# Kernel optimization log

Hardware: AMD Instinct MI355X
Metric: run time of the kernel (lower is better)

The kernel has to match this reference:

```python
import jax, jax.numpy as jnp
import numpy as np

NUM_NODES = 50000
FEAT_DIM = 64
HIDDEN = 128
OUT_DIM = 128
NUM_EDGES = 640000


def setup_inputs() -> dict:
    key = jax.random.key(0)
    ks = jax.random.split(key, 8)
    edge_index = jax.random.randint(ks[0], (2, NUM_EDGES), 0, NUM_NODES, dtype=jnp.int32)
    emb = jax.random.normal(ks[1], (NUM_NODES, FEAT_DIM), dtype=jnp.float32) * 0.1
    # SAGEConv: lin_l (aggregated neighbors, with bias) and lin_r (root, no bias)
    s1 = 1.0 / np.sqrt(FEAT_DIM)
    W1l = jax.random.uniform(ks[2], (HIDDEN, FEAT_DIM), jnp.float32, -s1, s1)
    b1l = jnp.zeros((HIDDEN,), jnp.float32)
    W1r = jax.random.uniform(ks[3], (HIDDEN, FEAT_DIM), jnp.float32, -s1, s1)
    s2 = 1.0 / np.sqrt(HIDDEN)
    W2l = jax.random.uniform(ks[4], (OUT_DIM, HIDDEN), jnp.float32, -s2, s2)
    b2l = jnp.zeros((OUT_DIM,), jnp.float32)
    W2r = jax.random.uniform(ks[5], (OUT_DIM, HIDDEN), jnp.float32, -s2, s2)
    return {"edge_index": edge_index, "emb": emb, "W1l": W1l, "b1l": b1l,
            "W1r": W1r, "W2l": W2l, "b2l": b2l, "W2r": W2r}


def _sage_conv(x, src, dst, Wl, bl, Wr):
    # mean-aggregate source features at target nodes, then two linear paths
    msg = x[src]                                   # [E, d]
    agg = jax.ops.segment_sum(msg, dst, num_segments=NUM_NODES)
    deg = jax.ops.segment_sum(jnp.ones((src.shape[0],), x.dtype), dst,
                              num_segments=NUM_NODES)
    mean = agg / jnp.maximum(deg, 1.0)[:, None]    # [N, d]
    return mean @ Wl.T + bl + x @ Wr.T             # [N, out]


def reference(edge_index, emb, W1l, b1l, W1r, W2l, b2l, W2r):
    src, dst = edge_index[0], edge_index[1]
    h = jax.nn.relu(_sage_conv(emb, src, dst, W1l, b1l, W1r))
    return _sage_conv(h, src, dst, W2l, b2l, W2r)
```

## Files before the change

### kernel.cpp

```cpp
#include <hip/hip_runtime.h>

#define N_NODES 50000
#define FEAT    64
#define HID     128
#define N_EDGES 640000
#define NBLK    196
#define GCAP    64

typedef __attribute__((ext_vector_type(8))) short bf16x8;
typedef __attribute__((ext_vector_type(4))) float f32x4;

static __device__ __forceinline__ unsigned short f2bf(float f) {
    unsigned u = __float_as_uint(f);
    u = u + 0x7fffu + ((u >> 16) & 1u);
    return (unsigned short)(u >> 16);
}
static __device__ __forceinline__ float bflo(unsigned u) {
    return __uint_as_float(u << 16);
}
static __device__ __forceinline__ float bfhi(unsigned u) {
    return __uint_as_float(u & 0xffff0000u);
}

#define ACC8(A, v) { \
    A[0] += bflo((v).x); A[1] += bfhi((v).x); \
    A[2] += bflo((v).y); A[3] += bfhi((v).y); \
    A[4] += bflo((v).z); A[5] += bfhi((v).z); \
    A[6] += bflo((v).w); A[7] += bfhi((v).w); }

static __device__ __forceinline__ void gridbar(int* bar, int gen) {
    __syncthreads();
    if (threadIdx.x == 0) {
        __threadfence();
        int arrived = atomicAdd(&bar[0], 1);
        if (arrived == NBLK - 1) {
            atomicExch(&bar[0], 0);
            __threadfence();
            atomicExch(&bar[1], gen);
        } else {
            while (atomicAdd(&bar[1], 0) < gen) __builtin_amdgcn_s_sleep(2);
        }
        __threadfence();
    }
    __syncthreads();
}

__global__ __launch_bounds__(256) void histcvt_kernel(
        const int* __restrict__ dst, const float* __restrict__ emb,
        const float* __restrict__ W1l, const float* __restrict__ W1r,
        const float* __restrict__ W2l, const float* __restrict__ W2r,
        int* __restrict__ count, int* __restrict__ eslot,
        unsigned* __restrict__ emb_bf_u, unsigned* __restrict__ Wbf_u,
        unsigned* __restrict__ hbf_u) {
    int gtid = blockIdx.x * 256 + threadIdx.x;
    if (gtid < N_EDGES) {
        int slot = atomicAdd(&count[dst[gtid]], 1);
        eslot[gtid] = slot;
    }
    for (int i = gtid; i < N_NODES * FEAT / 2; i += N_EDGES) {
        float2 v = ((const float2*)emb)[i];
        emb_bf_u[i] = ((unsigned)f2bf(v.y) << 16) | (unsigned)f2bf(v.x);
    }
    if (gtid < FEAT / 2) emb_bf_u[N_NODES * FEAT / 2 + gtid] = 0u;
    if (gtid < HID / 2)  hbf_u[N_NODES * HID / 2 + gtid]   = 0u;
    if (gtid < 24576) {
        int w = gtid * 2;
        float lo, hi;
        if (w < 8192)       { lo = W1l[w];         hi = W1l[w + 1]; }
        else if (w < 16384) { lo = W1r[w - 8192];  hi = W1r[w - 8191]; }
        else if (w < 32768) { lo = W2l[w - 16384]; hi = W2l[w - 16383]; }
        else                { lo = W2r[w - 32768]; hi = W2r[w - 32767]; }
        Wbf_u[gtid] = ((unsigned)f2bf(hi) << 16) | (unsigned)f2bf(lo);
    }
}

__global__ __launch_bounds__(256) void scanperm_kernel(
        const int* __restrict__ count, int* offset, int* dhist, int* dcur,
        int* bsum, int* boff, int* dstart, int* perm, int* bar) {
    __shared__ int tmp[256];
    __shared__ int lh[64];
    __shared__ int lb2[64];
    int t = threadIdx.x;
    int gtid = blockIdx.x * 256 + t;

    {
        if (t < 64) lh[t] = 0;
        int v = (gtid < N_NODES) ? count[gtid] : 0;
        tmp[t] = v;
        __syncthreads();
        if (gtid < N_NODES) atomicAdd(&lh[v < 63 ? v : 63], 1);
        for (int off = 1; off < 256; off <<= 1) {
            int add = (t >= off) ? tmp[t - off] : 0;
            __syncthreads();
            tmp[t] += add;
            __syncthreads();
        }
        if (gtid < N_NODES) offset[gtid] = tmp[t] - v;
        if (t == 255) bsum[blockIdx.x] = tmp[255];
        if (t < 64 && lh[t] > 0) atomicAdd(&dhist[t], lh[t]);
    }
    gridbar(bar, 1);

    if (blockIdx.x < 2) {
        const int* in  = (blockIdx.x == 0) ? bsum : dhist;
        int*       out = (blockIdx.x == 0) ? boff : dstart;
        int cnt        = (blockIdx.x == 0) ? NBLK : 64;
        int v = (t < cnt) ? in[t] : 0;
        tmp[t] = v;
        __syncthreads();
        for (int off = 1; off < 256; off <<= 1) {
            int add = (t >= off) ? tmp[t - off] : 0;
            __syncthreads();
            tmp[t] += add;
            __syncthreads();
        }
        if (t < cnt) out[t] = tmp[t] - v;
    }
    gridbar(bar, 2);

    if (gtid < N_NODES) offset[gtid] += boff[blockIdx.x];
    if (gtid == 0) offset[N_NODES] = N_EDGES;
    {
        if (t < 64) lh[t] = 0;
        __syncthreads();
        int d = 0, slot = 0;
        if (gtid < N_NODES) {
            int c = count[gtid];
            d = c < 63 ? c : 63;
            slot = atomicAdd(&lh[d], 1);
        }
        __syncthreads();
        if (t < 64 && lh[t] > 0) lb2[t] = atomicAdd(&dcur[t], lh[t]);
        __syncthreads();
        if (gtid < N_NODES)
            perm[(N_NODES - 1) - (dstart[d] + lb2[d] + slot)] = gtid;
    }
}

__global__ void fill_kernel(const int* __restrict__ src, const int* __restrict__ dst,
                            const int* __restrict__ offset,
                            const int* __restrict__ eslot, int* __restrict__ esrc) {
    int e = blockIdx.x * blockDim.x + threadIdx.x;
    if (e >= N_EDGES) return;
    esrc[offset[dst[e]] + eslot[e]] = src[e];
}

__global__ __launch_bounds__(256, 4) void fgemm1_kernel(
        const unsigned short* __restrict__ embb, const int* __restrict__ offset,
        const int* __restrict__ esrc, const int* __restrict__ perm,
        const short* __restrict__ Wl, const short* __restrict__ Wr,
        const float* __restrict__ bias, unsigned short* __restrict__ hout) {
    __shared__ unsigned short smean[16][72];
    __shared__ int sidx[16][GCAP];
    __shared__ int nid[16];
    int t = threadIdx.x;
    if (t < 16) nid[t] = perm[blockIdx.x * 16 + t];
    __syncthreads();

    int sub = t >> 4, fl = t & 15;
    int half = (t >> 3) & 1, fo = t & 7;
    int n = nid[sub];
    int beg = offset[n], deg = offset[n + 1] - beg;
    bool fast = deg <= GCAP;
    int rr = (deg + 15) & ~15;
    if (fast) {
        for (int j = fl; j < rr; j += 16)
            sidx[sub][j] = (j < deg) ? esrc[beg + j] : N_NODES;
    }
    float acc[8] = {0,0,0,0,0,0,0,0};
    const uint4* eb4 = (const uint4*)embb;
    if (fast) {
        for (int i = 0; i < rr; i += 16) {
            uint4 v0 = eb4[(size_t)sidx[sub][i +  0 + half] * 8 + fo];
            uint4 v1 = eb4[(size_t)sidx[sub][i +  2 + half] * 8 + fo];
            uint4 v2 = eb4[(size_t)sidx[sub][i +  4 + half] * 8 + fo];
            uint4 v3 = eb4[(size_t)sidx[sub][i +  6 + half] * 8 + fo];
            uint4 v4 = eb4[(size_t)sidx[sub][i +  8 + half] * 8 + fo];
            uint4 v5 = eb4[(size_t)sidx[sub][i + 10 + half] * 8 + fo];
            uint4 v6 = eb4[(size_t)sidx[sub][i + 12 + half] * 8 + fo];
            uint4 v7 = eb4[(size_t)sidx[sub][i + 14 + half] * 8 + fo];
            ACC8(acc, v0) ACC8(acc, v1) ACC8(acc, v2) ACC8(acc, v3)
            ACC8(acc, v4) ACC8(acc, v5) ACC8(acc, v6) ACC8(acc, v7)
        }
    } else {
        for (int i = half; i < deg; i += 2) {
            uint4 v = eb4[(size_t)esrc[beg + i] * 8 + fo];
            ACC8(acc, v)
        }
    }
    float dinv = 1.0f / fmaxf((float)deg, 1.0f);
    unsigned ow[4];
    #pragma unroll
    for (int k = 0; k < 4; ++k) {
        float lo = acc[2 * k];     lo += __shfl_xor(lo, 8);
        float hi = acc[2 * k + 1]; hi += __shfl_xor(hi, 8);
        ow[k] = ((unsigned)f2bf(hi * dinv) << 16) | (unsigned)f2bf(lo * dinv);
    }
    if (half == 0) {
        uint4 o4 = {ow[0], ow[1], ow[2], ow[3]};
        *(uint4*)&smean[sub][fo * 8] = o4;
    }
    __syncthreads();

    int wave = t >> 6, lane = t & 63;
    int col = lane & 15, quad = lane >> 4;
    int ncol = nid[col];
    int nt0 = wave * 2, nt1 = nt0 + 1;
    f32x4 acc0 = (f32x4){0.f,0.f,0.f,0.f}, acc1 = (f32x4){0.f,0.f,0.f,0.f};
    #pragma unroll
    for (int kb = 0; kb < FEAT; kb += 32) {
        bf16x8 am = *(const bf16x8*)&smean[col][kb + quad * 8];
        bf16x8 ax = *(const bf16x8*)(embb + (size_t)ncol * FEAT + kb + quad * 8);
        bf16x8 bl0 = *(const bf16x8*)(Wl + (nt0 * 16 + col) * FEAT + kb + quad * 8);
        bf16x8 br0 = *(const bf16x8*)(Wr + (nt0 * 16 + col) * FEAT + kb + quad * 8);
        bf16x8 bl1 = *(const bf16x8*)(Wl + (nt1 * 16 + col) * FEAT + kb + quad * 8);
        bf16x8 br1 = *(const bf16x8*)(Wr + (nt1 * 16 + col) * FEAT + kb + quad * 8);
        acc0 = __builtin_amdgcn_mfma_f32_16x16x32_bf16(am, bl0, acc0, 0, 0, 0);
        acc0 = __builtin_amdgcn_mfma_f32_16x16x32_bf16(ax, br0, acc0, 0, 0, 0);
        acc1 = __builtin_amdgcn_mfma_f32_16x16x32_bf16(am, bl1, acc1, 0, 0, 0);
        acc1 = __builtin_amdgcn_mfma_f32_16x16x32_bf16(ax, br1, acc1, 0, 0, 0);
    }
    float bv0 = bias[nt0 * 16 + col];
    float bv1 = bias[nt1 * 16 + col];
    #pragma unroll
    for (int r = 0; r < 4; ++r) {
        int node = nid[quad * 4 + r];
        hout[(size_t)node * HID + nt0 * 16 + col] = f2bf(fmaxf(acc0[r] + bv0, 0.f));
        hout[(size_t)node * HID + nt1 * 16 + col] = f2bf(fmaxf(acc1[r] + bv1, 0.f));
    }
}

__global__ __launch_bounds__(256, 4) void fgemm2_kernel(
        const unsigned short* __restrict__ hbf, const int* __restrict__ offset,
        const int* __restrict__ esrc, const int* __restrict__ perm,
        const short* __restrict__ Wl, const short* __restrict__ Wr,
        const float* __restrict__ bias, float* __restrict__ out) {
    __shared__ unsigned short smean[16][136];
    __shared__ int sidx[16][GCAP];
    __shared__ int nid[16];
    int t = threadIdx.x;
    if (t < 16) nid[t] = perm[blockIdx.x * 16 + t];
    __syncthreads();

    int sub = t >> 4, fl = t & 15;
    int n = nid[sub];
    int beg = offset[n], deg = offset[n + 1] - beg;
    bool fast = deg <= GCAP;
    int rr = (deg + 7) & ~7;
    if (fast) {
        for (int j = fl; j < rr; j += 16)
            sidx[sub][j] = (j < deg) ? esrc[beg + j] : N_NODES;
    }
    float acc[8] = {0,0,0,0,0,0,0,0};
    const uint4* hb4 = (const uint4*)hbf;
    if (fast) {
        for (int i = 0; i < rr; i += 8) {
            uint4 v0 = hb4[(size_t)sidx[sub][i + 0] * 16 + fl];
            uint4 v1 = hb4[(size_t)sidx[sub][i + 1] * 16 + fl];
            uint4 v2 = hb4[(size_t)sidx[sub][i + 2] * 16 + fl];
            uint4 v3 = hb4[(size_t)sidx[sub][i + 3] * 16 + fl];
            uint4 v4 = hb4[(size_t)sidx[sub][i + 4] * 16 + fl];
            uint4 v5 = hb4[(size_t)sidx[sub][i + 5] * 16 + fl];
            uint4 v6 = hb4[(size_t)sidx[sub][i + 6] * 16 + fl];
            uint4 v7 = hb4[(size_t)sidx[sub][i + 7] * 16 + fl];
            ACC8(acc, v0) ACC8(acc, v1) ACC8(acc, v2) ACC8(acc, v3)
            ACC8(acc, v4) ACC8(acc, v5) ACC8(acc, v6) ACC8(acc, v7)
        }
    } else {
        for (int i = 0; i < deg; ++i) {
            uint4 v = hb4[(size_t)esrc[beg + i] * 16 + fl];
            ACC8(acc, v)
        }
    }
    float dinv = 1.0f / fmaxf((float)deg, 1.0f);
    unsigned ow[4];
    #pragma unroll
    for (int k = 0; k < 4; ++k) {
        float lo = acc[2 * k] * dinv;
        float hi = acc[2 * k + 1] * dinv;
        ow[k] = ((unsigned)f2bf(hi) << 16) | (unsigned)f2bf(lo);
    }
    uint4 o4 = {ow[0], ow[1], ow[2], ow[3]};
    *(uint4*)&smean[sub][fl * 8] = o4;
    __syncthreads();

    int wave = t >> 6, lane = t & 63;
    int col = lane & 15, quad = lane >> 4;
    int ncol = nid[col];
    int nt0 = wave * 2, nt1 = nt0 + 1;
    f32x4 acc0 = (f32x4){0.f,0.f,0.f,0.f}, acc1 = (f32x4){0.f,0.f,0.f,0.f};
    #pragma unroll
    for (int kb = 0; kb < HID; kb += 32) {
        bf16x8 am = *(const bf16x8*)&smean[col][kb + quad * 8];
        bf16x8 ax = *(const bf16x8*)(hbf + (size_t)ncol * HID + kb + quad * 8);
        bf16x8 bl0 = *(const bf16x8*)(Wl + (nt0 * 16 + col) * HID + kb + quad * 8);
        bf16x8 br0 = *(const bf16x8*)(Wr + (nt0 * 16 + col) * HID + kb + quad * 8);
        bf16x8 bl1 = *(const bf16x8*)(Wl + (nt1 * 16 + col) * HID + kb + quad * 8);
        bf16x8 br1 = *(const bf16x8*)(Wr + (nt1 * 16 + col) * HID + kb + quad * 8);
        acc0 = __builtin_amdgcn_mfma_f32_16x16x32_bf16(am, bl0, acc0, 0, 0, 0);
        acc0 = __builtin_amdgcn_mfma_f32_16x16x32_bf16(ax, br0, acc0, 0, 0, 0);
        acc1 = __builtin_amdgcn_mfma_f32_16x16x32_bf16(am, bl1, acc1, 0, 0, 0);
        acc1 = __builtin_amdgcn_mfma_f32_16x16x32_bf16(ax, br1, acc1, 0, 0, 0);
    }
    float bv0 = bias[nt0 * 16 + col];
    float bv1 = bias[nt1 * 16 + col];
    #pragma unroll
    for (int r = 0; r < 4; ++r) {
        int node = nid[quad * 4 + r];
        out[(size_t)node * HID + nt0 * 16 + col] = acc0[r] + bv0;
        out[(size_t)node * HID + nt1 * 16 + col] = acc1[r] + bv1;
    }
}

extern "C" void kernel_launch(void* const* d_in, const int* in_sizes, int n_in,
                              void* d_out, int out_size, void* d_ws, size_t ws_size,
                              hipStream_t stream) {
    const int*   edge_index = (const int*)d_in[0];
    const float* emb        = (const float*)d_in[1];
    const float* W1l        = (const float*)d_in[2];
    const float* b1l        = (const float*)d_in[3];
    const float* W1r        = (const float*)d_in[4];
    const float* W2l        = (const float*)d_in[5];
    const float* b2l        = (const float*)d_in[6];
    const float* W2r        = (const float*)d_in[7];
    float* out = (float*)d_out;

    const int* src = edge_index;
    const int* dst = edge_index + N_EDGES;

    int* iws    = (int*)d_ws;
    int* offset = iws;
    int* count  = iws + 50004;
    int* dhist  = iws + 100004;
    int* dcur   = iws + 100068;
    int* bar    = iws + 100132;
    int* bsum   = iws + 100136;
    int* boff   = iws + 100392;
    int* dstart = iws + 100648;
    int* perm   = iws + 100712;
    int* esrc   = iws + 150712;
    int* eslot  = iws + 790712;
    unsigned short* W1l_bf = (unsigned short*)(iws + 1430712);
    unsigned short* W1r_bf = (unsigned short*)(iws + 1434808);
    unsigned short* W2l_bf = (unsigned short*)(iws + 1438904);
    unsigned short* W2r_bf = (unsigned short*)(iws + 1447096);
    unsigned short* Wbf    = W1l_bf;
    unsigned short* emb_bf = (unsigned short*)(iws + 1455288);
    unsigned short* hbf    = (unsigned short*)(iws + 3055320);

    (void)hipMemsetAsync(count, 0, (size_t)(100136 - 50004) * sizeof(int), stream);

    histcvt_kernel<<<(N_EDGES + 255) / 256, 256, 0, stream>>>(
        dst, emb, W1l, W1r, W2l, W2r, count, eslot,
        (unsigned*)emb_bf, (unsigned*)Wbf, (unsigned*)hbf);
    scanperm_kernel<<<NBLK, 256, 0, stream>>>(
        count, offset, dhist, dcur, bsum, boff, dstart, perm, bar);
    fill_kernel<<<(N_EDGES + 255) / 256, 256, 0, stream>>>(
        src, dst, offset, eslot, esrc);

    fgemm1_kernel<<<N_NODES / 16, 256, 0, stream>>>(
        emb_bf, offset, esrc, perm,
        (const short*)W1l_bf, (const short*)W1r_bf, b1l, hbf);
    fgemm2_kernel<<<N_NODES / 16, 256, 0, stream>>>(
        hbf, offset, esrc, perm,
        (const short*)W2l_bf, (const short*)W2r_bf, b2l, out);
}
```

Before: 230.5 us.

## Double-buffer neighbor gathers through LDS with async global_load_lds in both layers

Replaces the register-based unrolled neighbor gather in both fused SAGE kernels with a two-stage pipeline. It issues asynchronous global_load_lds transfers into a per-wave LDS staging buffer, waits with explicit vmcnt, and accumulates from LDS while the next batch is in flight. The fast-path decision now uses the wave-wide maximum degree, so all 16-lane groups in a wave share one loop trip count. The aim is to keep more gather loads outstanding and hide memory latency. The cost is extra LDS usage, manual waitcnt handling that could be fragile, and wasted padded loads when a wave's degrees are uneven.

```diff
diff --git a/kernel.cpp b/kernel.cpp
--- a/kernel.cpp
+++ b/kernel.cpp
@@ -27,6 +27,12 @@
     A[2] += bflo((v).y); A[3] += bfhi((v).y); \
     A[4] += bflo((v).z); A[5] += bfhi((v).z); \
     A[6] += bflo((v).w); A[7] += bfhi((v).w); }
+
+typedef __attribute__((address_space(1))) const void glob_void;
+typedef __attribute__((address_space(3))) void lds_void;
+static __device__ __forceinline__ void gload16(const void* g, void* l) {
+    __builtin_amdgcn_global_load_lds((glob_void*)g, (lds_void*)l, 16, 0, 0);
+}
 
 static __device__ __forceinline__ void gridbar(int* bar, int gen) {
     __syncthreads();
@@ -153,35 +159,60 @@
     __shared__ unsigned short smean[16][72];
     __shared__ int sidx[16][GCAP];
     __shared__ int nid[16];
+    __shared__ uint4 stg[4][2][4][4][2][8];
     int t = threadIdx.x;
     if (t < 16) nid[t] = perm[blockIdx.x * 16 + t];
     __syncthreads();
 
     int sub = t >> 4, fl = t & 15;
+    int w = t >> 6;
+    int subloc = sub & 3;
     int half = (t >> 3) & 1, fo = t & 7;
     int n = nid[sub];
     int beg = offset[n], deg = offset[n + 1] - beg;
-    bool fast = deg <= GCAP;
-    int rr = (deg + 15) & ~15;
-    if (fast) {
-        for (int j = fl; j < rr; j += 16)
-            sidx[sub][j] = (j < deg) ? esrc[beg + j] : N_NODES;
-    }
+    int degw = deg;
+    degw = max(degw, __shfl_xor(degw, 16));
+    degw = max(degw, __shfl_xor(degw, 32));
     float acc[8] = {0,0,0,0,0,0,0,0};
     const uint4* eb4 = (const uint4*)embb;
-    if (fast) {
-        for (int i = 0; i < rr; i += 16) {
-            uint4 v0 = eb4[(size_t)sidx[sub][i +  0 + half] * 8 + fo];
-            uint4 v1 = eb4[(size_t)sidx[sub][i +  2 + half] * 8 + fo];
-            uint4 v2 = eb4[(size_t)sidx[sub][i +  4 + half] * 8 + fo];
-            uint4 v3 = eb4[(size_t)sidx[sub][i +  6 + half] * 8 + fo];
-            uint4 v4 = eb4[(size_t)sidx[sub][i +  8 + half] * 8 + fo];
-            uint4 v5 = eb4[(size_t)sidx[sub][i + 10 + half] * 8 + fo];
-            uint4 v6 = eb4[(size_t)sidx[sub][i + 12 + half] * 8 + fo];
-            uint4 v7 = eb4[(size_t)sidx[sub][i + 14 + half] * 8 + fo];
-            ACC8(acc, v0) ACC8(acc, v1) ACC8(acc, v2) ACC8(acc, v3)
-            ACC8(acc, v4) ACC8(acc, v5) ACC8(acc, v6) ACC8(acc, v7)
-        }
+
+    if (degw <= GCAP) {
+        int rrw = (degw + 7) & ~7;
+        for (int j = fl; j < rrw; j += 16)
+            sidx[sub][j] = (j < deg) ? esrc[beg + j] : N_NODES;
+        int nw = rrw >> 3;
+
+#define ISSUE1(k, buf) { \
+        int rb = (k) * 8; \
+        _Pragma("unroll") \
+        for (int j = 0; j < 4; ++j) { \
+            const uint4* g = eb4 + (size_t)sidx[(w<<2) + subloc][rb + j*2 + half] * 8 + fo; \
+            gload16(g, &stg[w][buf][j][0][0][0]); \
+        } }
+#define CONSUME1(buf) { \
+        _Pragma("unroll") \
+        for (int j = 0; j < 4; ++j) { \
+            uint4 v = stg[w][buf][j][subloc][half][fo]; \
+            ACC8(acc, v) \
+        } }
+
+        if (nw > 0) {
+            ISSUE1(0, 0)
+            if (nw > 1) ISSUE1(1, 1)
+            for (int k = 0; k < nw; ++k) {
+                if (k < nw - 1) { asm volatile("s_waitcnt vmcnt(4)" ::: "memory"); }
+                else            { asm volatile("s_waitcnt vmcnt(0)" ::: "memory"); }
+                __builtin_amdgcn_sched_barrier(0);
+                if (k & 1) { CONSUME1(1) } else { CONSUME1(0) }
+                if (k + 2 < nw) {
+                    asm volatile("s_waitcnt lgkmcnt(0)" ::: "memory");
+                    __builtin_amdgcn_sched_barrier(0);
+                    if (k & 1) { ISSUE1(k + 2, 1) } else { ISSUE1(k + 2, 0) }
+                }
+            }
+        }
+#undef ISSUE1
+#undef CONSUME1
     } else {
         for (int i = half; i < deg; i += 2) {
             uint4 v = eb4[(size_t)esrc[beg + i] * 8 + fo];
@@ -238,34 +269,59 @@
     __shared__ unsigned short smean[16][136];
     __shared__ int sidx[16][GCAP];
     __shared__ int nid[16];
+    __shared__ uint4 stg[4][2][4][4][16];
     int t = threadIdx.x;
     if (t < 16) nid[t] = perm[blockIdx.x * 16 + t];
     __syncthreads();
 
     int sub = t >> 4, fl = t & 15;
+    int w = t >> 6;
+    int subloc = sub & 3;
     int n = nid[sub];
     int beg = offset[n], deg = offset[n + 1] - beg;
-    bool fast = deg <= GCAP;
-    int rr = (deg + 7) & ~7;
-    if (fast) {
-        for (int j = fl; j < rr; j += 16)
-            sidx[sub][j] = (j < deg) ? esrc[beg + j] : N_NODES;
-    }
+    int degw = deg;
+    degw = max(degw, __shfl_xor(degw, 16));
+    degw = max(degw, __shfl_xor(degw, 32));
     float acc[8] = {0,0,0,0,0,0,0,0};
     const uint4* hb4 = (const uint4*)hbf;
-    if (fast) {
-        for (int i = 0; i < rr; i += 8) {
-            uint4 v0 = hb4[(size_t)sidx[sub][i + 0] * 16 + fl];
-            uint4 v1 = hb4[(size_t)sidx[sub][i + 1] * 16 + fl];
-            uint4 v2 = hb4[(size_t)sidx[sub][i + 2] * 16 + fl];
-            uint4 v3 = hb4[(size_t)sidx[sub][i + 3] * 16 + fl];
-            uint4 v4 = hb4[(size_t)sidx[sub][i + 4] * 16 + fl];
-            uint4 v5 = hb4[(size_t)sidx[sub][i + 5] * 16 + fl];
-            uint4 v6 = hb4[(size_t)sidx[sub][i + 6] * 16 + fl];
-            uint4 v7 = hb4[(size_t)sidx[sub][i + 7] * 16 + fl];
-            ACC8(acc, v0) ACC8(acc, v1) ACC8(acc, v2) ACC8(acc, v3)
-            ACC8(acc, v4) ACC8(acc, v5) ACC8(acc, v6) ACC8(acc, v7)
-        }
+
+    if (degw <= GCAP) {
+        int rrw = (degw + 3) & ~3;
+        for (int j = fl; j < rrw; j += 16)
+            sidx[sub][j] = (j < deg) ? esrc[beg + j] : N_NODES;
+        int nw = rrw >> 2;
+
+#define ISSUE2(k, buf) { \
+        int rb = (k) * 4; \
+        _Pragma("unroll") \
+        for (int j = 0; j < 4; ++j) { \
+            const uint4* g = hb4 + (size_t)sidx[(w<<2) + subloc][rb + j] * 16 + fl; \
+            gload16(g, &stg[w][buf][j][0][0]); \
+        } }
+#define CONSUME2(buf) { \
+        _Pragma("unroll") \
+        for (int j = 0; j < 4; ++j) { \
+            uint4 v = stg[w][buf][j][subloc][fl]; \
+            ACC8(acc, v) \
+        } }
+
+        if (nw > 0) {
+            ISSUE2(0, 0)
+            if (nw > 1) ISSUE2(1, 1)
+            for (int k = 0; k < nw; ++k) {
+                if (k < nw - 1) { asm volatile("s_waitcnt vmcnt(4)" ::: "memory"); }
+                else            { asm volatile("s_waitcnt vmcnt(0)" ::: "memory"); }
+                __builtin_amdgcn_sched_barrier(0);
+                if (k & 1) { CONSUME2(1) } else { CONSUME2(0) }
+                if (k + 2 < nw) {
+                    asm volatile("s_waitcnt lgkmcnt(0)" ::: "memory");
+                    __builtin_amdgcn_sched_barrier(0);
+                    if (k & 1) { ISSUE2(k + 2, 1) } else { ISSUE2(k + 2, 0) }
+                }
+            }
+        }
+#undef ISSUE2
+#undef CONSUME2
     } else {
         for (int i = 0; i < deg; ++i) {
             uint4 v = hb4[(size_t)esrc[beg + i] * 16 + fl];
```

After: 237.4 us. +3.0%, slower.

## Bucket edges with a cursor atomic and split GEMM kernels into interleaved halves

Applied to the files above, without the earlier changes.

The histogram no longer stores a per-edge slot. The scan writes a per-node cursor array, and the fill kernel takes slots from it with atomics, which removes the eslot write and read traffic. Each fused gather+GEMM layer is now launched twice, once for even and once for odd 16-node groups of the degree-sorted permutation. This appears to aim at load balance or tail behaviour across launches. The cost is an extra kernel launch per layer, and neighbour order within each CSR row becomes nondeterministic.

```diff
diff --git a/kernel.cpp b/kernel.cpp
--- a/kernel.cpp
+++ b/kernel.cpp
@@ -49,13 +49,12 @@
         const int* __restrict__ dst, const float* __restrict__ emb,
         const float* __restrict__ W1l, const float* __restrict__ W1r,
         const float* __restrict__ W2l, const float* __restrict__ W2r,
-        int* __restrict__ count, int* __restrict__ eslot,
+        int* __restrict__ count,
         unsigned* __restrict__ emb_bf_u, unsigned* __restrict__ Wbf_u,
         unsigned* __restrict__ hbf_u) {
     int gtid = blockIdx.x * 256 + threadIdx.x;
     if (gtid < N_EDGES) {
-        int slot = atomicAdd(&count[dst[gtid]], 1);
-        eslot[gtid] = slot;
+        atomicAdd(&count[dst[gtid]], 1);
     }
     for (int i = gtid; i < N_NODES * FEAT / 2; i += N_EDGES) {
         float2 v = ((const float2*)emb)[i];
@@ -75,8 +74,8 @@
 }
 
 __global__ __launch_bounds__(256) void scanperm_kernel(
-        const int* __restrict__ count, int* offset, int* dhist, int* dcur,
-        int* bsum, int* boff, int* dstart, int* perm, int* bar) {
+        const int* __restrict__ count, int* offset, int* cur, int* dhist,
+        int* dcur, int* bsum, int* boff, int* dstart, int* perm, int* bar) {
     __shared__ int tmp[256];
     __shared__ int lh[64];
     __shared__ int lb2[64];
@@ -118,7 +117,11 @@
     }
     gridbar(bar, 2);
 
-    if (gtid < N_NODES) offset[gtid] += boff[blockIdx.x];
+    if (gtid < N_NODES) {
+        int o = offset[gtid] + boff[blockIdx.x];
+        offset[gtid] = o;
+        cur[gtid] = o;
+    }
     if (gtid == 0) offset[N_NODES] = N_EDGES;
     {
         if (t < 64) lh[t] = 0;
@@ -138,23 +141,25 @@
 }
 
 __global__ void fill_kernel(const int* __restrict__ src, const int* __restrict__ dst,
-                            const int* __restrict__ offset,
-                            const int* __restrict__ eslot, int* __restrict__ esrc) {
+                            int* __restrict__ cur, int* __restrict__ esrc) {
     int e = blockIdx.x * blockDim.x + threadIdx.x;
     if (e >= N_EDGES) return;
-    esrc[offset[dst[e]] + eslot[e]] = src[e];
+    int slot = atomicAdd(&cur[dst[e]], 1);
+    esrc[slot] = src[e];
 }
 
 __global__ __launch_bounds__(256, 4) void fgemm1_kernel(
         const unsigned short* __restrict__ embb, const int* __restrict__ offset,
         const int* __restrict__ esrc, const int* __restrict__ perm,
         const short* __restrict__ Wl, const short* __restrict__ Wr,
-        const float* __restrict__ bias, unsigned short* __restrict__ hout) {
+        const float* __restrict__ bias, unsigned short* __restrict__ hout,
+        int pblk) {
     __shared__ unsigned short smean[16][72];
     __shared__ int sidx[16][GCAP];
     __shared__ int nid[16];
     int t = threadIdx.x;
-    if (t < 16) nid[t] = perm[blockIdx.x * 16 + t];
+    int pb = blockIdx.x * 2 + pblk;
+    if (t < 16) nid[t] = perm[pb * 16 + t];
     __syncthreads();
 
     int sub = t >> 4, fl = t & 15;
@@ -234,12 +239,14 @@
         const unsigned short* __restrict__ hbf, const int* __restrict__ offset,
         const int* __restrict__ esrc, const int* __restrict__ perm,
         const short* __restrict__ Wl, const short* __restrict__ Wr,
-        const float* __restrict__ bias, float* __restrict__ out) {
+        const float* __restrict__ bias, float* __restrict__ out,
+        int pblk) {
     __shared__ unsigned short smean[16][136];
     __shared__ int sidx[16][GCAP];
     __shared__ int nid[16];
     int t = threadIdx.x;
-    if (t < 16) nid[t] = perm[blockIdx.x * 16 + t];
+    int pb = blockIdx.x * 2 + pblk;
+    if (t < 16) nid[t] = perm[pb * 16 + t];
     __syncthreads();
 
     int sub = t >> 4, fl = t & 15;
@@ -339,7 +346,7 @@
     int* dstart = iws + 100648;
     int* perm   = iws + 100712;
     int* esrc   = iws + 150712;
-    int* eslot  = iws + 790712;
+    int* cur    = iws + 790712;
     unsigned short* W1l_bf = (unsigned short*)(iws + 1430712);
     unsigned short* W1r_bf = (unsigned short*)(iws + 1434808);
     unsigned short* W2l_bf = (unsigned short*)(iws + 1438904);
@@ -351,17 +358,24 @@
     (void)hipMemsetAsync(count, 0, (size_t)(100136 - 50004) * sizeof(int), stream);
 
     histcvt_kernel<<<(N_EDGES + 255) / 256, 256, 0, stream>>>(
-        dst, emb, W1l, W1r, W2l, W2r, count, eslot,
+        dst, emb, W1l, W1r, W2l, W2r, count,
         (unsigned*)emb_bf, (unsigned*)Wbf, (unsigned*)hbf);
     scanperm_kernel<<<NBLK, 256, 0, stream>>>(
-        count, offset, dhist, dcur, bsum, boff, dstart, perm, bar);
+        count, offset, cur, dhist, dcur, bsum, boff, dstart, perm, bar);
     fill_kernel<<<(N_EDGES + 255) / 256, 256, 0, stream>>>(
-        src, dst, offset, eslot, esrc);
-
-    fgemm1_kernel<<<N_NODES / 16, 256, 0, stream>>>(
+        src, dst, cur, esrc);
+
+    fgemm1_kernel<<<1563, 256, 0, stream>>>(
         emb_bf, offset, esrc, perm,
-        (const short*)W1l_bf, (const short*)W1r_bf, b1l, hbf);
-    fgemm2_kernel<<<N_NODES / 16, 256, 0, stream>>>(
+        (const short*)W1l_bf, (const short*)W1r_bf, b1l, hbf, 0);
+    fgemm1_kernel<<<1562, 256, 0, stream>>>(
+        emb_bf, offset, esrc, perm,
+        (const short*)W1l_bf, (const short*)W1r_bf, b1l, hbf, 1);
+
+    fgemm2_kernel<<<1563, 256, 0, stream>>>(
         hbf, offset, esrc, perm,
-        (const short*)W2l_bf, (const short*)W2r_bf, b2l, out);
-}
+        (const short*)W2l_bf, (const short*)W2r_bf, b2l, out, 0);
+    fgemm2_kernel<<<1562, 256, 0, stream>>>(
+        hbf, offset, esrc, perm,
+        (const short*)W2l_bf, (const short*)W2r_bf, b2l, out, 1);
+}
```

Result: slower. 267.1 us (+15.9%).

## Fuse histogram, scan, permutation and CSR fill into one persistent kernel

Applied to the files above, without the earlier changes.

Merges the histogram/convert, scan/permutation and fill kernels into a single persistent 1024-block kernel that uses software grid barriers between phases, removing two kernel launches. The CSR fill now claims slots with a second atomic on a per-node cursor instead of storing and reloading per-edge slot indices, which saves the eslot write and read. The cost is four grid-wide barriers across 1024 blocks, a cooperative-residency assumption (1024 blocks at 4 per CU must all be resident), and a nondeterministic edge order within each node.

```diff
diff --git a/kernel.cpp b/kernel.cpp
--- a/kernel.cpp
+++ b/kernel.cpp
@@ -4,7 +4,8 @@
 #define FEAT    64
 #define HID     128
 #define N_EDGES 640000
-#define NBLK    196
+#define PBLK    1024
+#define SBLK    196
 #define GCAP    64
 
 typedef __attribute__((ext_vector_type(8))) short bf16x8;
@@ -28,12 +29,12 @@
     A[4] += bflo((v).z); A[5] += bfhi((v).z); \
     A[6] += bflo((v).w); A[7] += bfhi((v).w); }
 
-static __device__ __forceinline__ void gridbar(int* bar, int gen) {
+static __device__ __forceinline__ void gridbar(int* bar, int gen, int nblk) {
     __syncthreads();
     if (threadIdx.x == 0) {
         __threadfence();
         int arrived = atomicAdd(&bar[0], 1);
-        if (arrived == NBLK - 1) {
+        if (arrived == nblk - 1) {
             atomicExch(&bar[0], 0);
             __threadfence();
             atomicExch(&bar[1], gen);
@@ -45,19 +46,25 @@
     __syncthreads();
 }
 
-__global__ __launch_bounds__(256) void histcvt_kernel(
-        const int* __restrict__ dst, const float* __restrict__ emb,
+__global__ __launch_bounds__(256, 4) void prep_kernel(
+        const int* __restrict__ src, const int* __restrict__ dst,
+        const float* __restrict__ emb,
         const float* __restrict__ W1l, const float* __restrict__ W1r,
         const float* __restrict__ W2l, const float* __restrict__ W2r,
-        int* __restrict__ count, int* __restrict__ eslot,
+        int* __restrict__ count, int* offset, int* cur, int* dhist, int* dcur,
+        int* bsum, int* boff, int* dstart, int* perm, int* esrc, int* bar,
         unsigned* __restrict__ emb_bf_u, unsigned* __restrict__ Wbf_u,
         unsigned* __restrict__ hbf_u) {
-    int gtid = blockIdx.x * 256 + threadIdx.x;
-    if (gtid < N_EDGES) {
-        int slot = atomicAdd(&count[dst[gtid]], 1);
-        eslot[gtid] = slot;
-    }
-    for (int i = gtid; i < N_NODES * FEAT / 2; i += N_EDGES) {
+    __shared__ int tmp[256];
+    __shared__ int lh[64];
+    __shared__ int lb2[64];
+    int t = threadIdx.x;
+    int gtid = blockIdx.x * 256 + t;
+    const int GRID = PBLK * 256;
+
+    for (int e = gtid; e < N_EDGES; e += GRID)
+        atomicAdd(&count[dst[e]], 1);
+    for (int i = gtid; i < N_NODES * FEAT / 2; i += GRID) {
         float2 v = ((const float2*)emb)[i];
         emb_bf_u[i] = ((unsigned)f2bf(v.y) << 16) | (unsigned)f2bf(v.x);
     }
@@ -72,18 +79,9 @@
         else                { lo = W2r[w - 32768]; hi = W2r[w - 32767]; }
         Wbf_u[gtid] = ((unsigned)f2bf(hi) << 16) | (unsigned)f2bf(lo);
     }
-}
-
-__global__ __launch_bounds__(256) void scanperm_kernel(
-        const int* __restrict__ count, int* offset, int* dhist, int* dcur,
-        int* bsum, int* boff, int* dstart, int* perm, int* bar) {
-    __shared__ int tmp[256];
-    __shared__ int lh[64];
-    __shared__ int lb2[64];
-    int t = threadIdx.x;
-    int gtid = blockIdx.x * 256 + t;
-
-    {
+    gridbar(bar, 1, PBLK);
+
+    if (blockIdx.x < SBLK) {
         if (t < 64) lh[t] = 0;
         int v = (gtid < N_NODES) ? count[gtid] : 0;
         tmp[t] = v;
@@ -99,12 +97,12 @@
         if (t == 255) bsum[blockIdx.x] = tmp[255];
         if (t < 64 && lh[t] > 0) atomicAdd(&dhist[t], lh[t]);
     }
-    gridbar(bar, 1);
+    gridbar(bar, 2, PBLK);
 
     if (blockIdx.x < 2) {
         const int* in  = (blockIdx.x == 0) ? bsum : dhist;
         int*       out = (blockIdx.x == 0) ? boff : dstart;
-        int cnt        = (blockIdx.x == 0) ? NBLK : 64;
+        int cnt        = (blockIdx.x == 0) ? SBLK : 64;
         int v = (t < cnt) ? in[t] : 0;
         tmp[t] = v;
         __syncthreads();
@@ -116,11 +114,15 @@
         }
         if (t < cnt) out[t] = tmp[t] - v;
     }
-    gridbar(bar, 2);
-
-    if (gtid < N_NODES) offset[gtid] += boff[blockIdx.x];
-    if (gtid == 0) offset[N_NODES] = N_EDGES;
-    {
+    gridbar(bar, 3, PBLK);
+
+    if (blockIdx.x < SBLK) {
+        if (gtid < N_NODES) {
+            int o = offset[gtid] + boff[blockIdx.x];
+            offset[gtid] = o;
+            cur[gtid] = o;
+        }
+        if (gtid == 0) offset[N_NODES] = N_EDGES;
         if (t < 64) lh[t] = 0;
         __syncthreads();
         int d = 0, slot = 0;
@@ -135,14 +137,12 @@
         if (gtid < N_NODES)
             perm[(N_NODES - 1) - (dstart[d] + lb2[d] + slot)] = gtid;
     }
-}
-
-__global__ void fill_kernel(const int* __restrict__ src, const int* __restrict__ dst,
-                            const int* __restrict__ offset,
-                            const int* __restrict__ eslot, int* __restrict__ esrc) {
-    int e = blockIdx.x * blockDim.x + threadIdx.x;
-    if (e >= N_EDGES) return;
-    esrc[offset[dst[e]] + eslot[e]] = src[e];
+    gridbar(bar, 4, PBLK);
+
+    for (int e = gtid; e < N_EDGES; e += GRID) {
+        int slot = atomicAdd(&cur[dst[e]], 1);
+        esrc[slot] = src[e];
+    }
 }
 
 __global__ __launch_bounds__(256, 4) void fgemm1_kernel(
@@ -339,7 +339,7 @@
     int* dstart = iws + 100648;
     int* perm   = iws + 100712;
     int* esrc   = iws + 150712;
-    int* eslot  = iws + 790712;
+    int* cur    = iws + 790712;
     unsigned short* W1l_bf = (unsigned short*)(iws + 1430712);
     unsigned short* W1r_bf = (unsigned short*)(iws + 1434808);
     unsigned short* W2l_bf = (unsigned short*)(iws + 1438904);
@@ -350,13 +350,10 @@
 
     (void)hipMemsetAsync(count, 0, (size_t)(100136 - 50004) * sizeof(int), stream);
 
-    histcvt_kernel<<<(N_EDGES + 255) / 256, 256, 0, stream>>>(
-        dst, emb, W1l, W1r, W2l, W2r, count, eslot,
+    prep_kernel<<<PBLK, 256, 0, stream>>>(
+        src, dst, emb, W1l, W1r, W2l, W2r,
+        count, offset, cur, dhist, dcur, bsum, boff, dstart, perm, esrc, bar,
         (unsigned*)emb_bf, (unsigned*)Wbf, (unsigned*)hbf);
-    scanperm_kernel<<<NBLK, 256, 0, stream>>>(
-        count, offset, dhist, dcur, bsum, boff, dstart, perm, bar);
-    fill_kernel<<<(N_EDGES + 255) / 256, 256, 0, stream>>>(
-        src, dst, offset, eslot, esrc);
 
     fgemm1_kernel<<<N_NODES / 16, 256, 0, stream>>>(
         emb_bf, offset, esrc, perm,
```

After: 523.1 us. 127% more time.
